# Kernel optimization log

Hardware: AMD Instinct MI355X
Metric: run time of the kernel (lower is better)

## Reference

```python
import jax, jax.numpy as jnp
import numpy as np

B, T, C, HS = 8, 4096, 1024, 128
BLOCK = 4096  # block_size; T == BLOCK here


def _pyr_mask(bs):
    # Faithful numpy translation of the torch 'pyr' buffer construction.
    h = bs // 2
    top = np.repeat(np.flip(np.tril(np.ones((h, h), np.float32)), axis=1), 2, axis=0)  # (bs, h)
    reps = np.array([2] * (h - 1) + [1])
    bot = np.concatenate(
        [np.zeros((1, h), np.float32),
         np.repeat(np.tril(np.ones((h, h), np.float32)), reps, axis=0)], axis=0)  # (bs, h)
    return np.concatenate([top, bot], axis=1)  # (bs, bs)


def setup_inputs() -> dict:
    key = jax.random.key(0)
    kx, kq, kk, kv = jax.random.split(key, 4)
    s = C ** -0.5
    x = jax.random.normal(kx, (B, T, C), jnp.float32)
    Wq = jax.random.normal(kq, (C, HS), jnp.float32) * s
    Wk = jax.random.normal(kk, (C, HS), jnp.float32) * s
    Wv = jax.random.normal(kv, (C, HS), jnp.float32) * s
    return {"x": x, "Wq": Wq, "Wk": Wk, "Wv": Wv}


def reference(x, Wq, Wk, Wv):
    Tlen = x.shape[1]
    start = (BLOCK - Tlen) // 2
    end = BLOCK + (-(BLOCK - Tlen)) // 2  # python floor-div, matches torch slicing
    mask = jnp.asarray(_pyr_mask(BLOCK)[:Tlen, start:end])  # (T, T) 0/1

    q = x @ Wq  # (B, T, HS)
    k = x @ Wk
    v = x @ Wv
    wei = jnp.einsum('btd,bsd->bts', q, k) * (HS ** -0.5)  # (B, T, T)
    wei = jnp.where(mask == 0, -jnp.inf, wei)  # bidirectional_mode == 'bi'
    wei = jax.nn.softmax(wei, axis=-1)
    # dropout p=0.0 -> identity
    return wei @ v  # (B, T, HS)
```

## Files before the change

### kernel.cpp

```cpp
#include <hip/hip_runtime.h>

typedef unsigned short u16;
typedef __attribute__((ext_vector_type(8))) short bf16x8;
typedef __attribute__((ext_vector_type(8))) unsigned short u16x8;
typedef __attribute__((ext_vector_type(4))) float f32x4;
typedef __attribute__((ext_vector_type(4))) unsigned short u16x4;
typedef __attribute__((ext_vector_type(2))) unsigned int u32x2;
typedef __attribute__((ext_vector_type(4))) unsigned int u32x4;

#define Bn 8
#define Tn 4096
#define Cn 1024
#define HSn 128

__device__ __forceinline__ float bf2f(u16 b) {
    unsigned u = ((unsigned)b) << 16;
    return __builtin_bit_cast(float, u);
}
__device__ __forceinline__ unsigned cvt_pk_bf16(float a, float b) {
    unsigned r;
    asm("v_cvt_pk_bf16_f32 %0, %1, %2" : "=v"(r) : "v"(a), "v"(b));
    return r;
}
__device__ __forceinline__ u16 f2bf(float f) { return (u16)cvt_pk_bf16(f, f); }

__device__ __forceinline__ void wg_barrier() {
    __builtin_amdgcn_sched_barrier(0);
    asm volatile("s_waitcnt lgkmcnt(0)" ::: "memory");
    __builtin_amdgcn_s_barrier();
    __builtin_amdgcn_sched_barrier(0);
}

extern "C" __global__ __launch_bounds__(256) void head_wtrans(
    const float* __restrict__ Wq, const float* __restrict__ Wk,
    const float* __restrict__ Wv, u16* __restrict__ wt) {
    const float* W = (blockIdx.y == 0) ? Wq : (blockIdx.y == 1) ? Wk : Wv;
    const float scale =
        (blockIdx.y == 0) ? (0.08838834764831845f * 1.4426950408889634f) : 1.0f;
    u16* o = wt + (size_t)blockIdx.y * Cn * HSn;
    int tid = blockIdx.x * 256 + threadIdx.x;
    int n = tid >> 10, kk = tid & 1023;
    o[tid] = f2bf(W[kk * HSn + n] * scale);
}

extern "C" __global__ __launch_bounds__(256, 1) void head_proj(
    const float* __restrict__ x, const u16* __restrict__ wt, u16* __restrict__ qo,
    u16* __restrict__ ko, u16* __restrict__ vto) {
    __shared__ __align__(16) u16 tL[128 * 80];
    const int tid = threadIdx.x;
    const int w = tid >> 6, l = tid & 63, quad = l >> 4, ln = l & 15;
    const int bm0 = blockIdx.x * 64;
    const int m0w = (w & 1) * 32, n0w = (w >> 1) * 64;

    const f32x4 zero4 = {0.f, 0.f, 0.f, 0.f};
    f32x4 acc[3][2][4];
#pragma unroll
    for (int s = 0; s < 3; s++)
#pragma unroll
        for (int i = 0; i < 2; i++)
#pragma unroll
            for (int j = 0; j < 4; j++) acc[s][i][j] = zero4;

    const float* xp0 = x + ((size_t)(bm0 + m0w + ln)) * Cn + quad * 8;
    const float* xp1 = xp0 + (size_t)16 * Cn;
    const u16* wbase = wt + ((size_t)(n0w + ln)) * Cn + quad * 8;

#define PROJ_LOADX(XC, KT)                             \
    do {                                               \
        XC[0][0] = *(const f32x4*)(xp0 + (KT) * 32);   \
        XC[0][1] = *(const f32x4*)(xp0 + (KT) * 32 + 4); \
        XC[1][0] = *(const f32x4*)(xp1 + (KT) * 32);   \
        XC[1][1] = *(const f32x4*)(xp1 + (KT) * 32 + 4); \
    } while (0)

#define PROJ_LOADW(WB, KT)                                                  \
    do {                                                                    \
        _Pragma("unroll") for (int s = 0; s < 3; s++)                       \
            _Pragma("unroll") for (int ni = 0; ni < 4; ni++)                \
                WB[s * 4 + ni] = *(const u16x8*)(wbase + (size_t)s * (Cn * HSn) + \
                                                 ni * (16 * Cn) + (KT) * 32);     \
    } while (0)

#define PROJ_COMPUTE(XC, WB)                                                   \
    do {                                                                       \
        bf16x8 af[2];                                                          \
        _Pragma("unroll") for (int mi = 0; mi < 2; mi++) {                     \
            u32x4 t;                                                          \
            t[0] = cvt_pk_bf16(XC[mi][0][0], XC[mi][0][1]);                    \
            t[1] = cvt_pk_bf16(XC[mi][0][2], XC[mi][0][3]);                    \
            t[2] = cvt_pk_bf16(XC[mi][1][0], XC[mi][1][1]);                    \
            t[3] = cvt_pk_bf16(XC[mi][1][2], XC[mi][1][3]);                    \
            af[mi] = __builtin_bit_cast(bf16x8, t);                            \
        }                                                                      \
        _Pragma("unroll") for (int s = 0; s < 3; s++)                          \
            _Pragma("unroll") for (int mi = 0; mi < 2; mi++)                   \
                _Pragma("unroll") for (int ni = 0; ni < 4; ni++)               \
                    acc[s][mi][ni] = __builtin_amdgcn_mfma_f32_16x16x32_bf16(  \
                        af[mi], __builtin_bit_cast(bf16x8, WB[s * 4 + ni]),    \
                        acc[s][mi][ni], 0, 0, 0);                              \
    } while (0)

    f32x4 xA[2][2], xB[2][2];
    u16x8 wb[12];
    PROJ_LOADX(xA, 0);
    for (int kt = 0; kt < 32; kt += 2) {
        PROJ_LOADW(wb, kt);
        PROJ_LOADX(xB, kt + 1);
        PROJ_COMPUTE(xA, wb);
        PROJ_LOADW(wb, kt + 1);
        if (kt + 2 < 32) PROJ_LOADX(xA, kt + 2);
        PROJ_COMPUTE(xB, wb);
    }
#undef PROJ_LOADX
#undef PROJ_LOADW
#undef PROJ_COMPUTE

#pragma unroll
    for (int mi = 0; mi < 2; mi++)
#pragma unroll
        for (int ni = 0; ni < 4; ni++)
#pragma unroll
            for (int r = 0; r < 4; r++) {
                int grow = bm0 + m0w + mi * 16 + quad * 4 + r;
                int col = n0w + ni * 16 + ln;
                qo[(size_t)grow * HSn + col] = f2bf(acc[0][mi][ni][r]);
                ko[(size_t)grow * HSn + col] = f2bf(acc[1][mi][ni][r]);
            }
#pragma unroll
    for (int mi = 0; mi < 2; mi++)
#pragma unroll
        for (int ni = 0; ni < 4; ni++) {
            int col = n0w + ni * 16 + ln;
            int trow0 = m0w + mi * 16 + quad * 4;
            u16x4 pk4;
#pragma unroll
            for (int r = 0; r < 4; r++) pk4[r] = f2bf(acc[2][mi][ni][r]);
            *(u16x4*)(tL + col * 80 + trow0) = pk4;
        }
    wg_barrier();
    {
        const int bb = bm0 >> 12, t0b = bm0 & 4095;
        const int dl = tid >> 3, tch = (tid & 7) * 8;
#pragma unroll
        for (int db = 0; db < 4; db++) {
            int d = db * 32 + dl;
            u16x8 vv = *(const u16x8*)(tL + d * 80 + tch);
            *(u16x8*)(vto + ((size_t)bb * HSn + d) * Tn + t0b + tch) = vv;
        }
    }
}

extern "C" __global__ __launch_bounds__(512) void head_flash_chunk(
    const u16* __restrict__ q, const u16* __restrict__ k, const u16* __restrict__ vt,
    u16* __restrict__ Opart, float* __restrict__ lsum) {
    __shared__ __align__(16) u16 kL[64 * 136];
    __shared__ __align__(16) u16 vL[128 * 72];
    __shared__ __align__(16) u16 pL[8 * 16 * 72];
    const int tid = threadIdx.x;
    const int w = tid >> 6, l = tid & 63, quad = l >> 4, ln = l & 15;
    const int cid = blockIdx.x;
    const int grp = cid >> 4;
    const int qbi = (grp < 16) ? (31 - grp) : (grp - 16);
    const int b = (cid >> 1) & 7;
    const int half = cid & 1;
    const int q0 = qbi * 128;
    const int qrow = q0 + w * 16;

    const int rkBase = tid >> 4, ckK = tid & 15;
    const int rvBase = tid >> 3, ckV = tid & 7;

    bf16x8 qf[4];
#pragma unroll
    for (int ks = 0; ks < 4; ks++)
        qf[ks] = *(const bf16x8*)(q + ((size_t)b * Tn + qrow + ln) * HSn + ks * 32 +
                                  quad * 8);

    const f32x4 zero4 = {0.f, 0.f, 0.f, 0.f};
    float l2 = 0.f;
    const int qme = qrow + ln;
    const int clo = 2047 - (qme >> 1), chi = 2047 + ((qme + 1) >> 1);
    const int cloW0 = 2047 - (qrow >> 1);
    const int chiW0 = 2047 + ((qrow + 1) >> 1);
    const int cloMin = 2047 - ((qrow + 15) >> 1);
    const int chiMax = 2047 + ((qrow + 16) >> 1);
    f32x4 o[8];
#pragma unroll
    for (int dt = 0; dt < 8; dt++) o[dt] = zero4;

    const int qmax = q0 + 127;
    const int tlo = (2047 - (qmax >> 1)) >> 6;
    const int thi = (2047 + ((qmax + 1) >> 1)) >> 6;
    const int W = thi - tlo + 1;
    const int c0 = (W + 1) >> 1;
    const int kstart = half ? tlo + c0 : tlo;
    const int kend = half ? thi : tlo + c0 - 1;

    u16x8 pk[2], pv[2];
    {
        const int t0 = kstart * 64;
#pragma unroll
        for (int p = 0; p < 2; p++)
            pk[p] = *(const u16x8*)(k + ((size_t)b * Tn + t0 + p * 32 + rkBase) * HSn +
                                    ckK * 8);
#pragma unroll
        for (int p = 0; p < 2; p++)
            pv[p] = *(const u16x8*)(vt + ((size_t)b * HSn + p * 64 + rvBase) * Tn + t0 +
                                    ckV * 8);
    }

    for (int kt = kstart; kt <= kend; kt++) {
        const int t0 = kt * 64;
        wg_barrier();
#pragma unroll
        for (int p = 0; p < 2; p++)
            *(u16x8*)(kL + (p * 32 + rkBase) * 136 + ckK * 8) = pk[p];
#pragma unroll
        for (int p = 0; p < 2; p++)
            *(u16x8*)(vL + (p * 64 + rvBase) * 72 + ckV * 8) = pv[p];
        if (kt < kend) {
            const int t1 = t0 + 64;
#pragma unroll
            for (int p = 0; p < 2; p++)
                pk[p] = *(const u16x8*)(k + ((size_t)b * Tn + t1 + p * 32 + rkBase) * HSn +
                                        ckK * 8);
#pragma unroll
            for (int p = 0; p < 2; p++)
                pv[p] = *(const u16x8*)(vt + ((size_t)b * HSn + p * 64 + rvBase) * Tn +
                                        t1 + ckV * 8);
        }
        wg_barrier();

        const bool live = !((t0 + 63 < cloMin) || (t0 > chiMax));

        if (live) {
            f32x4 s[4];
#pragma unroll
            for (int nt = 0; nt < 4; nt++) s[nt] = zero4;
            __builtin_amdgcn_s_setprio(1);
#pragma unroll
            for (int nt = 0; nt < 4; nt++) {
                int R = nt * 16 + ln;
#pragma unroll
                for (int ks = 0; ks < 4; ks++) {
                    bf16x8 kf = *(const bf16x8*)(kL + R * 136 + (ks * 4 + quad) * 8);
                    s[nt] =
                        __builtin_amdgcn_mfma_f32_16x16x32_bf16(kf, qf[ks], s[nt], 0, 0, 0);
                }
            }
            __builtin_amdgcn_s_setprio(0);
            if (t0 < cloW0 || t0 + 63 > chiW0) {
#pragma unroll
                for (int nt = 0; nt < 4; nt++)
#pragma unroll
                    for (int r = 0; r < 4; r++) {
                        int t = t0 + nt * 16 + quad * 4 + r;
                        bool valid = (t >= clo) && (t <= chi);
                        s[nt][r] = valid ? s[nt][r] : -1e30f;
                    }
            }
            float ls = 0.f;
#pragma unroll
            for (int nt = 0; nt < 4; nt++) {
                float p0 = exp2f(s[nt][0]), p1 = exp2f(s[nt][1]);
                float p2 = exp2f(s[nt][2]), p3 = exp2f(s[nt][3]);
                ls += (p0 + p1) + (p2 + p3);
                u32x2 d;
                d.x = cvt_pk_bf16(p0, p1);
                d.y = cvt_pk_bf16(p2, p3);
                *(u32x2*)(pL + w * 1152 + ln * 72 + nt * 16 + quad * 4) = d;
            }
            l2 += ls;
            __builtin_amdgcn_s_setprio(1);
#pragma unroll
            for (int jt = 0; jt < 2; jt++) {
                bf16x8 pf = *(const bf16x8*)(pL + w * 1152 + ln * 72 + jt * 32 + quad * 8);
#pragma unroll
                for (int dt = 0; dt < 8; dt++) {
                    int R = dt * 16 + ln;
                    bf16x8 vf = *(const bf16x8*)(vL + R * 72 + (jt * 4 + quad) * 8);
                    o[dt] = __builtin_amdgcn_mfma_f32_16x16x32_bf16(pf, vf, o[dt], 0, 0, 0);
                }
            }
            __builtin_amdgcn_s_setprio(0);
        }
    }
    l2 += __shfl_xor(l2, 16, 64);
    l2 += __shfl_xor(l2, 32, 64);
#pragma unroll
    for (int dt = 0; dt < 8; dt++)
#pragma unroll
        for (int r = 0; r < 4; r++)
            Opart[((size_t)cid * 128 + w * 16 + quad * 4 + r) * HSn + dt * 16 + ln] =
                f2bf(o[dt][r]);
    if (l < 16) lsum[(size_t)cid * 128 + w * 16 + ln] = l2;
}

extern "C" __global__ __launch_bounds__(256) void head_combine(
    const u16* __restrict__ Opart, const float* __restrict__ lsum,
    float* __restrict__ out) {
    const int bid = blockIdx.x;
    const int qb64 = bid >> 3, b = bid & 7;
    const int tid = threadIdx.x;
    const int row = tid >> 2, dseg = (tid & 3) * 32;
    const int qbi = qb64 >> 1;
    const int inrow = (qb64 & 1) * 64 + row;
    const int grp0 = (qbi >= 16) ? (31 - qbi) : (qbi + 16);
    const int cid0 = grp0 * 16 + b * 2;
    const size_t r0 = (size_t)cid0 * 128 + inrow, r1 = r0 + 128;
    float l0 = lsum[r0], l1 = lsum[r1];
    float inv = 1.0f / (l0 + l1);
    float* op = out + ((size_t)b * Tn + qb64 * 64 + row) * HSn + dseg;
    const u16* p0 = Opart + r0 * HSn + dseg;
    const u16* p1 = Opart + r1 * HSn + dseg;
#pragma unroll
    for (int j = 0; j < 4; j++) {
        u16x8 a = *(const u16x8*)(p0 + j * 8);
        u16x8 c = *(const u16x8*)(p1 + j * 8);
        f32x4 o1, o2;
#pragma unroll
        for (int e = 0; e < 4; e++) o1[e] = (bf2f(a[e]) + bf2f(c[e])) * inv;
#pragma unroll
        for (int e = 0; e < 4; e++) o2[e] = (bf2f(a[4 + e]) + bf2f(c[4 + e])) * inv;
        *(f32x4*)(op + j * 8) = o1;
        *(f32x4*)(op + j * 8 + 4) = o2;
    }
}

extern "C" __global__ __launch_bounds__(256) void head_flash(
    const u16* __restrict__ q, const u16* __restrict__ k, const u16* __restrict__ vt,
    float* __restrict__ out) {
    __shared__ __align__(16) u16 kL[64 * 136];
    __shared__ __align__(16) u16 vL[128 * 72];
    __shared__ __align__(16) u16 pL[4 * 16 * 72];
    const int tid = threadIdx.x;
    const int w = tid >> 6, l = tid & 63, quad = l >> 4, ln = l & 15;
    const int bx = blockIdx.x;
    const int half = bx >> 8, idx = bx & 255;
    const int p5 = idx & 31, b = idx >> 5;
    const int qb = half ? p5 : 63 - p5;
    const int q0 = qb * 64;
    const int qrow = q0 + w * 16;
    const int rkBase = tid >> 4, ckK = tid & 15;
    const int rvBase = tid >> 3, ckV = tid & 7;

    bf16x8 qf[4];
#pragma unroll
    for (int ks = 0; ks < 4; ks++)
        qf[ks] = *(const bf16x8*)(q + ((size_t)b * Tn + qrow + ln) * HSn + ks * 32 +
                                  quad * 8);
    const f32x4 zero4 = {0.f, 0.f, 0.f, 0.f};
    float m2 = -1e30f, l2 = 0.f;
    const int qme = qrow + ln;
    const int clo = 2047 - (qme >> 1), chi = 2047 + ((qme + 1) >> 1);
    f32x4 o[8];
#pragma unroll
    for (int dt = 0; dt < 8; dt++) o[dt] = zero4;
    const int qmax = q0 + 63;
    const int tlo = (2047 - (qmax >> 1)) >> 6;
    const int thi = (2047 + ((qmax + 1) >> 1)) >> 6;

    u16x8 pk[4], pv[4];
    {
        const int t0 = tlo * 64;
#pragma unroll
        for (int p = 0; p < 4; p++)
            pk[p] = *(const u16x8*)(k + ((size_t)b * Tn + t0 + p * 16 + rkBase) * HSn +
                                    ckK * 8);
#pragma unroll
        for (int p = 0; p < 4; p++)
            pv[p] = *(const u16x8*)(vt + ((size_t)b * HSn + p * 32 + rvBase) * Tn + t0 +
                                    ckV * 8);
    }
    for (int kt = tlo; kt <= thi; kt++) {
        const int t0 = kt * 64;
        __syncthreads();
#pragma unroll
        for (int p = 0; p < 4; p++)
            *(u16x8*)(kL + (p * 16 + rkBase) * 136 + ckK * 8) = pk[p];
#pragma unroll
        for (int p = 0; p < 4; p++)
            *(u16x8*)(vL + (p * 32 + rvBase) * 72 + ckV * 8) = pv[p];
        if (kt < thi) {
            const int t1 = t0 + 64;
#pragma unroll
            for (int p = 0; p < 4; p++)
                pk[p] = *(const u16x8*)(k + ((size_t)b * Tn + t1 + p * 16 + rkBase) * HSn +
                                        ckK * 8);
#pragma unroll
            for (int p = 0; p < 4; p++)
                pv[p] = *(const u16x8*)(vt + ((size_t)b * HSn + p * 32 + rvBase) * Tn +
                                        t1 + ckV * 8);
        }
        __syncthreads();
        f32x4 s[4];
#pragma unroll
        for (int nt = 0; nt < 4; nt++) s[nt] = zero4;
#pragma unroll
        for (int nt = 0; nt < 4; nt++) {
            int R = nt * 16 + ln;
#pragma unroll
            for (int ks = 0; ks < 4; ks++) {
                bf16x8 kf = *(const bf16x8*)(kL + R * 136 + (ks * 4 + quad) * 8);
                s[nt] = __builtin_amdgcn_mfma_f32_16x16x32_bf16(kf, qf[ks], s[nt], 0, 0, 0);
            }
        }
#pragma unroll
        for (int nt = 0; nt < 4; nt++)
#pragma unroll
            for (int r = 0; r < 4; r++) {
                int t = t0 + nt * 16 + quad * 4 + r;
                bool valid = (t >= clo) && (t <= chi);
                s[nt][r] = valid ? s[nt][r] : -1e30f;
            }
        float mc = s[0][0];
#pragma unroll
        for (int nt = 0; nt < 4; nt++)
#pragma unroll
            for (int r = 0; r < 4; r++) mc = fmaxf(mc, s[nt][r]);
        mc = fmaxf(mc, __shfl_xor(mc, 16, 64));
        mc = fmaxf(mc, __shfl_xor(mc, 32, 64));
        float mn = fmaxf(m2, mc);
        float alpha = exp2f(m2 - mn);
        m2 = mn;
        float ls = 0.f;
#pragma unroll
        for (int nt = 0; nt < 4; nt++) {
            float p0 = exp2f(s[nt][0] - mn), p1 = exp2f(s[nt][1] - mn);
            float p2 = exp2f(s[nt][2] - mn), p3 = exp2f(s[nt][3] - mn);
            ls += (p0 + p1) + (p2 + p3);
            u32x2 d;
            d.x = cvt_pk_bf16(p0, p1);
            d.y = cvt_pk_bf16(p2, p3);
            *(u32x2*)(pL + w * 1152 + ln * 72 + nt * 16 + quad * 4) = d;
        }
        ls += __shfl_xor(ls, 16, 64);
        ls += __shfl_xor(ls, 32, 64);
        l2 = l2 * alpha + ls;
        float aR[4];
#pragma unroll
        for (int r = 0; r < 4; r++) aR[r] = __shfl(alpha, quad * 4 + r, 64);
#pragma unroll
        for (int dt = 0; dt < 8; dt++) {
            f32x4 oo = o[dt];
#pragma unroll
            for (int r = 0; r < 4; r++) oo[r] *= aR[r];
            o[dt] = oo;
        }
#pragma unroll
        for (int jt = 0; jt < 2; jt++) {
            bf16x8 pf = *(const bf16x8*)(pL + w * 1152 + ln * 72 + jt * 32 + quad * 8);
#pragma unroll
            for (int dt = 0; dt < 8; dt++) {
                int R = dt * 16 + ln;
                bf16x8 vf = *(const bf16x8*)(vL + R * 72 + (jt * 4 + quad) * 8);
                o[dt] = __builtin_amdgcn_mfma_f32_16x16x32_bf16(pf, vf, o[dt], 0, 0, 0);
            }
        }
    }
    float inv = 1.0f / l2;
    float rl[4];
#pragma unroll
    for (int r = 0; r < 4; r++) rl[r] = __shfl(inv, quad * 4 + r, 64);
#pragma unroll
    for (int dt = 0; dt < 8; dt++)
#pragma unroll
        for (int r = 0; r < 4; r++) {
            int row = qrow + quad * 4 + r;
            out[((size_t)b * Tn + row) * HSn + dt * 16 + ln] = o[dt][r] * rl[r];
        }
}

extern "C" void kernel_launch(void* const* d_in, const int* in_sizes, int n_in,
                              void* d_out, int out_size, void* d_ws, size_t ws_size,
                              hipStream_t stream) {
    const float* x = (const float*)d_in[0];
    const float* Wq = (const float*)d_in[1];
    const float* Wk = (const float*)d_in[2];
    const float* Wv = (const float*)d_in[3];
    float* outp = (float*)d_out;
    char* ws = (char*)d_ws;
    u16* wt = (u16*)(ws);
    u16* qb = (u16*)(ws + (1u << 20));
    u16* kb = (u16*)(ws + (9u << 20));
    u16* vtb = (u16*)(ws + (17u << 20));
    u16* Opart = (u16*)(ws + (25u << 20));
    float* lsum = (float*)(ws + (42u << 20));

    head_wtrans<<<dim3(512, 3), 256, 0, stream>>>(Wq, Wk, Wv, wt);
    head_proj<<<dim3(512), 256, 0, stream>>>(x, wt, qb, kb, vtb);
    if (ws_size >= (44ull << 20)) {
        head_flash_chunk<<<dim3(512), 512, 0, stream>>>(qb, kb, vtb, Opart, lsum);
        head_combine<<<dim3(512), 256, 0, stream>>>(Opart, lsum, outp);
    } else {
        head_flash<<<dim3(512), 256, 0, stream>>>(qb, kb, vtb, outp);
    }
}
```

Measured before the change: 365.4 us.

## Stage projection GEMM operands through LDS with async global-to-LDS loads

The QKV projection kernel now loads its x and weight tiles into a double-buffered 64KB shared-memory region using global_load_lds DMA with XOR swizzling. Before, each wave read its operands directly from global memory into registers, so waves sharing a tile loaded it redundantly. Each wave now reads MFMA fragments from LDS. The launch bound drops the min-blocks hint. In exchange this adds barriers and vmcnt(0) waits per k-step, and 64KB of LDS limits occupancy.

```diff
diff --git a/kernel.cpp b/kernel.cpp
--- a/kernel.cpp
+++ b/kernel.cpp
@@ -29,6 +29,12 @@
     asm volatile("s_waitcnt lgkmcnt(0)" ::: "memory");
     __builtin_amdgcn_s_barrier();
     __builtin_amdgcn_sched_barrier(0);
+}
+
+__device__ __forceinline__ void dma16(const void* g, void* l) {
+    __builtin_amdgcn_global_load_lds(
+        (const __attribute__((address_space(1))) unsigned int*)g,
+        (__attribute__((address_space(3))) unsigned int*)l, 16, 0, 0);
 }
 
 extern "C" __global__ __launch_bounds__(256) void head_wtrans(
@@ -43,10 +49,10 @@
     o[tid] = f2bf(W[kk * HSn + n] * scale);
 }
 
-extern "C" __global__ __launch_bounds__(256, 1) void head_proj(
+extern "C" __global__ __launch_bounds__(256) void head_proj(
     const float* __restrict__ x, const u16* __restrict__ wt, u16* __restrict__ qo,
     u16* __restrict__ ko, u16* __restrict__ vto) {
-    __shared__ __align__(16) u16 tL[128 * 80];
+    __shared__ __align__(16) unsigned char sh[65536];
     const int tid = threadIdx.x;
     const int w = tid >> 6, l = tid & 63, quad = l >> 4, ln = l & 15;
     const int bm0 = blockIdx.x * 64;
@@ -61,58 +67,65 @@
 #pragma unroll
             for (int j = 0; j < 4; j++) acc[s][i][j] = zero4;
 
-    const float* xp0 = x + ((size_t)(bm0 + m0w + ln)) * Cn + quad * 8;
-    const float* xp1 = xp0 + (size_t)16 * Cn;
-    const u16* wbase = wt + ((size_t)(n0w + ln)) * Cn + quad * 8;
-
-#define PROJ_LOADX(XC, KT)                             \
-    do {                                               \
-        XC[0][0] = *(const f32x4*)(xp0 + (KT) * 32);   \
-        XC[0][1] = *(const f32x4*)(xp0 + (KT) * 32 + 4); \
-        XC[1][0] = *(const f32x4*)(xp1 + (KT) * 32);   \
-        XC[1][1] = *(const f32x4*)(xp1 + (KT) * 32 + 4); \
+    const int gsx = ((tid & 7) ^ ((tid >> 3) & 7)) * 4;
+    const float* xsrc0 = x + (size_t)(bm0 + (tid >> 3)) * Cn + gsx;
+    const float* xsrc1 = xsrc0 + (size_t)32 * Cn;
+    const int gw = ((tid & 3) ^ ((tid >> 2) & 3)) * 8;
+    const u16* pw[6];
+#pragma unroll
+    for (int c = 0; c < 6; c++)
+        pw[c] = wt + (size_t)(c >> 1) * (Cn * HSn) +
+                (size_t)((c & 1) * 64 + (tid >> 2)) * Cn + gw;
+
+    const int aoff0 = (m0w + ln) * 128 + (((2 * quad) ^ (ln & 7)) * 16);
+    const int woff0 = (n0w + ln) * 64 + ((quad ^ (ln & 3)) * 16);
+
+#define PROJ_STAGE(BASE, KT)                                                     \
+    do {                                                                         \
+        dma16(xsrc0 + (KT) * 32, sh + (BASE) + tid * 16);                        \
+        dma16(xsrc1 + (KT) * 32, sh + (BASE) + 4096 + tid * 16);                 \
+        _Pragma("unroll") for (int c = 0; c < 6; c++)                            \
+            dma16(pw[c] + (KT) * 32, sh + (BASE) + 8192 + c * 4096 + tid * 16);  \
     } while (0)
 
-#define PROJ_LOADW(WB, KT)                                                  \
-    do {                                                                    \
-        _Pragma("unroll") for (int s = 0; s < 3; s++)                       \
-            _Pragma("unroll") for (int ni = 0; ni < 4; ni++)                \
-                WB[s * 4 + ni] = *(const u16x8*)(wbase + (size_t)s * (Cn * HSn) + \
-                                                 ni * (16 * Cn) + (KT) * 32);     \
+#define PROJ_COMPUTE(BASE)                                                       \
+    do {                                                                         \
+        const unsigned char* xb = sh + (BASE);                                   \
+        const unsigned char* wbp = sh + (BASE) + 8192;                           \
+        bf16x8 af[2];                                                            \
+        _Pragma("unroll") for (int mi = 0; mi < 2; mi++) {                       \
+            f32x4 lo = *(const f32x4*)(xb + (aoff0 + mi * 2048));                \
+            f32x4 hi = *(const f32x4*)(xb + ((aoff0 ^ 16) + mi * 2048));         \
+            u32x4 tt;                                                            \
+            tt[0] = cvt_pk_bf16(lo[0], lo[1]);                                   \
+            tt[1] = cvt_pk_bf16(lo[2], lo[3]);                                   \
+            tt[2] = cvt_pk_bf16(hi[0], hi[1]);                                   \
+            tt[3] = cvt_pk_bf16(hi[2], hi[3]);                                   \
+            af[mi] = __builtin_bit_cast(bf16x8, tt);                             \
+        }                                                                        \
+        _Pragma("unroll") for (int s = 0; s < 3; s++)                            \
+            _Pragma("unroll") for (int ni = 0; ni < 4; ni++) {                   \
+                bf16x8 bf = *(const bf16x8*)(wbp + (woff0 + s * 8192 + ni * 1024)); \
+                _Pragma("unroll") for (int mi = 0; mi < 2; mi++)                 \
+                    acc[s][mi][ni] = __builtin_amdgcn_mfma_f32_16x16x32_bf16(    \
+                        af[mi], bf, acc[s][mi][ni], 0, 0, 0);                    \
+            }                                                                    \
     } while (0)
 
-#define PROJ_COMPUTE(XC, WB)                                                   \
-    do {                                                                       \
-        bf16x8 af[2];                                                          \
-        _Pragma("unroll") for (int mi = 0; mi < 2; mi++) {                     \
-            u32x4 t;                                                          \
-            t[0] = cvt_pk_bf16(XC[mi][0][0], XC[mi][0][1]);                    \
-            t[1] = cvt_pk_bf16(XC[mi][0][2], XC[mi][0][3]);                    \
-            t[2] = cvt_pk_bf16(XC[mi][1][0], XC[mi][1][1]);                    \
-            t[3] = cvt_pk_bf16(XC[mi][1][2], XC[mi][1][3]);                    \
-            af[mi] = __builtin_bit_cast(bf16x8, t);                            \
-        }                                                                      \
-        _Pragma("unroll") for (int s = 0; s < 3; s++)                          \
-            _Pragma("unroll") for (int mi = 0; mi < 2; mi++)                   \
-                _Pragma("unroll") for (int ni = 0; ni < 4; ni++)               \
-                    acc[s][mi][ni] = __builtin_amdgcn_mfma_f32_16x16x32_bf16(  \
-                        af[mi], __builtin_bit_cast(bf16x8, WB[s * 4 + ni]),    \
-                        acc[s][mi][ni], 0, 0, 0);                              \
-    } while (0)
-
-    f32x4 xA[2][2], xB[2][2];
-    u16x8 wb[12];
-    PROJ_LOADX(xA, 0);
+    PROJ_STAGE(0, 0);
+    asm volatile("s_waitcnt vmcnt(0)" ::: "memory");
+    wg_barrier();
     for (int kt = 0; kt < 32; kt += 2) {
-        PROJ_LOADW(wb, kt);
-        PROJ_LOADX(xB, kt + 1);
-        PROJ_COMPUTE(xA, wb);
-        PROJ_LOADW(wb, kt + 1);
-        if (kt + 2 < 32) PROJ_LOADX(xA, kt + 2);
-        PROJ_COMPUTE(xB, wb);
-    }
-#undef PROJ_LOADX
-#undef PROJ_LOADW
+        PROJ_STAGE(32768, kt + 1);
+        PROJ_COMPUTE(0);
+        asm volatile("s_waitcnt vmcnt(0)" ::: "memory");
+        wg_barrier();
+        if (kt + 2 < 32) PROJ_STAGE(0, kt + 2);
+        PROJ_COMPUTE(32768);
+        asm volatile("s_waitcnt vmcnt(0)" ::: "memory");
+        wg_barrier();
+    }
+#undef PROJ_STAGE
 #undef PROJ_COMPUTE
 
 #pragma unroll
@@ -126,6 +139,7 @@
                 qo[(size_t)grow * HSn + col] = f2bf(acc[0][mi][ni][r]);
                 ko[(size_t)grow * HSn + col] = f2bf(acc[1][mi][ni][r]);
             }
+    u16* const tL = (u16*)sh;
 #pragma unroll
     for (int mi = 0; mi < 2; mi++)
 #pragma unroll
```

Result: faster. 298.8 us (-18.2%).
